# Kernel optimization log

Hardware: AMD Instinct MI355X
Metric: run time of the kernel (lower is better)

The kernel has to match this reference:

```python
import jax, jax.numpy as jnp
import numpy as np

N_NODES = 100000
N_EDGES = 1600000
F_IN, F_HID, F_OUT = 128, 128, 40


def setup_inputs() -> dict:
    key = jax.random.key(0)
    ks = jax.random.split(key, 8)
    x = jax.random.normal(ks[0], (N_NODES, F_IN), dtype=jnp.float32)
    edge_index = jax.random.randint(ks[1], (2, N_EDGES), 0, N_NODES, dtype=jnp.int64)
    # GCNConv weights (glorot-style scale); biases zero per bias_init=zeros_
    W0 = jax.random.normal(ks[2], (F_IN, F_HID), dtype=jnp.float32) / np.sqrt(F_IN)
    b0 = jnp.zeros((F_HID,), dtype=jnp.float32)
    W1 = jax.random.normal(ks[3], (F_HID, F_HID), dtype=jnp.float32) / np.sqrt(F_HID)
    b1 = jnp.zeros((F_HID,), dtype=jnp.float32)
    W2 = jax.random.normal(ks[4], (F_HID, F_OUT), dtype=jnp.float32) / np.sqrt(F_HID)
    b2 = jnp.zeros((F_OUT,), dtype=jnp.float32)
    return {"x": x, "edge_index": edge_index, "W0": W0, "b0": b0,
            "W1": W1, "b1": b1, "W2": W2, "b2": b2}


def _gcn_conv(h, src, dst, W, b):
    # PyG GCNConv (normalize=False, add_self_loops=False):
    # linear transform, then sum-aggregate source features at destinations.
    h = h @ W                                   # [N, F_out]
    msgs = jnp.take(h, src, axis=0)             # [E, F_out] gather
    agg = jax.ops.segment_sum(msgs, dst, num_segments=N_NODES)  # scatter-add
    return agg + b


def reference(x, edge_index, W0, b0, W1, b1, W2, b2):
    src, dst = edge_index[0], edge_index[1]     # flow: source -> target
    h = jax.nn.relu(_gcn_conv(x, src, dst, W0, b0))
    h = jax.nn.relu(_gcn_conv(h, src, dst, W1, b1))
    out = _gcn_conv(h, src, dst, W2, b2)        # last layer: no activation
    return out
```

## Files before the change

### kernel.cpp

```cpp
#include <hip/hip_runtime.h>


typedef short bf16x8 __attribute__((ext_vector_type(8)));
typedef float f32x4  __attribute__((ext_vector_type(4)));

#define EPB 4096

__device__ __forceinline__ float bflo(unsigned int v) {
  union { float f; unsigned int i; } w; w.i = v << 16; return w.f;
}
__device__ __forceinline__ float bfhi(unsigned int v) {
  union { float f; unsigned int i; } w; w.i = v & 0xffff0000u; return w.f;
}
__device__ __forceinline__ unsigned short f2bf(float f) {
  union { float f; unsigned int i; } w; w.f = f;
  unsigned int b = w.i;
  unsigned int r = (b + 0x7fffu + ((b >> 16) & 1u)) >> 16;
  return (unsigned short)r;
}

__device__ __forceinline__ int edge_at(const void* ei, int is64, long long pos) {
  if (is64) return (int)((const long long*)ei)[pos];
  return ((const int*)ei)[pos];
}

__global__ void k_detect(const int* __restrict__ ei32, int* __restrict__ flag) {
  int tid = threadIdx.x;
  int v = ei32[2 * tid + 1];
  unsigned long long m = __ballot(v != 0);
  if (tid == 0) flag[0] = (m == 0ull) ? 1 : 0;
}

__global__ void k_cvt(const float* __restrict__ in, unsigned short* __restrict__ out,
                      long long n4) {
  long long i = (long long)blockIdx.x * blockDim.x + threadIdx.x;
  if (i >= n4) return;
  float4 v = *reinterpret_cast<const float4*>(in + i * 4);
  ushort4 o;
  o.x = f2bf(v.x); o.y = f2bf(v.y); o.z = f2bf(v.z); o.w = f2bf(v.w);
  *reinterpret_cast<ushort4*>(out + i * 4) = o;
}

__global__ void k_wt3(const float* __restrict__ W0, const float* __restrict__ W1,
                      const float* __restrict__ W2,
                      unsigned short* __restrict__ Wt0, unsigned short* __restrict__ Wt1,
                      unsigned short* __restrict__ Wt2, int FOUT, int FP3) {
  int idx = blockIdx.x * blockDim.x + threadIdx.x;
  if (idx < 16384) {
    int c = idx >> 7, k = idx & 127;
    Wt0[c * 128 + k] = f2bf(W0[k * 128 + c]);
  } else if (idx < 32768) {
    int t = idx - 16384;
    int c = t >> 7, k = t & 127;
    Wt1[c * 128 + k] = f2bf(W1[k * 128 + c]);
  } else {
    int t = idx - 32768;
    if (t < FP3 * 128) {
      int c = t >> 7, k = t & 127;
      Wt2[c * 128 + k] = (c < FOUT) ? f2bf(W2[k * FOUT + c]) : (unsigned short)0;
    }
  }
}

__global__ __launch_bounds__(256) void b_hist(const void* __restrict__ ei,
                                              const int* __restrict__ flag, int E,
                                              int* __restrict__ bhist,
                                              int NBKT, int NBLKE) {
  __shared__ int h[512];
  int blk = blockIdx.x, tid = threadIdx.x;
  for (int i = tid; i < NBKT; i += 256) h[i] = 0;
  __syncthreads();
  int is64 = flag[0];
  int base = blk * EPB;
  int cnt = min(EPB, E - base);
  for (int i = tid; i < cnt; i += 256) {
    int d = edge_at(ei, is64, (long long)E + base + i);
    atomicAdd(&h[d >> 8], 1);
  }
  __syncthreads();
  for (int i = tid; i < NBKT; i += 256) bhist[i * NBLKE + blk] = h[i];
}

__global__ void k_scan_a(const int* __restrict__ vals, int* __restrict__ lscan,
                         int* __restrict__ partials, int n) {
  __shared__ int sm[256];
  int tid = threadIdx.x;
  int i = blockIdx.x * 256 + tid;
  int v = (i < n) ? vals[i] : 0;
  sm[tid] = v;
  __syncthreads();
  for (int off = 1; off < 256; off <<= 1) {
    int t = (tid >= off) ? sm[tid - off] : 0;
    __syncthreads();
    sm[tid] += t;
    __syncthreads();
  }
  if (i < n) lscan[i] = sm[tid];
  if (tid == 255) partials[blockIdx.x] = sm[255];
}

__global__ void k_scan_b(int* __restrict__ partials, int nb) {
  __shared__ int sm[1024];
  int tid = threadIdx.x;
  int v = (tid < nb) ? partials[tid] : 0;
  sm[tid] = v;
  __syncthreads();
  for (int off = 1; off < 1024; off <<= 1) {
    int t = (tid >= off) ? sm[tid - off] : 0;
    __syncthreads();
    sm[tid] += t;
    __syncthreads();
  }
  if (tid < nb) partials[tid] = sm[tid] - v;
}

__global__ void k_scan_c(const int* __restrict__ lscan, const int* __restrict__ vals,
                         const int* __restrict__ partials, int* __restrict__ scanned,
                         int* __restrict__ bucketPtr, int n, int NBLKE, int NBKT, int E) {
  int i = blockIdx.x * 256 + threadIdx.x;
  if (i >= n) return;
  int v = lscan[i] - vals[i] + partials[blockIdx.x];
  scanned[i] = v;
  int q = i / NBLKE;
  if (i - q * NBLKE == 0) bucketPtr[q] = v;
  if (i == 0) bucketPtr[NBKT] = E;
}

__global__ __launch_bounds__(256) void b_scatter(const void* __restrict__ ei,
                                                 const int* __restrict__ flag, int E,
                                                 const int* __restrict__ scanned,
                                                 uint2* __restrict__ ebuf,
                                                 int NBKT, int NBLKE) {
  __shared__ int base[512];
  int blk = blockIdx.x, tid = threadIdx.x;
  for (int i = tid; i < NBKT; i += 256) base[i] = scanned[i * NBLKE + blk];
  __syncthreads();
  int is64 = flag[0];
  int b0 = blk * EPB;
  int cnt = min(EPB, E - b0);
  for (int i = tid; i < cnt; i += 256) {
    int d = edge_at(ei, is64, (long long)E + b0 + i);
    int s = edge_at(ei, is64, b0 + i);
    int pos = atomicAdd(&base[d >> 8], 1);
    ebuf[pos] = make_uint2((unsigned)d, (unsigned)s);
  }
}

__global__ __launch_bounds__(256) void b_pass2(const uint2* __restrict__ ebuf,
                                               const int* __restrict__ bucketPtr,
                                               int* __restrict__ rowptr,
                                               int* __restrict__ colsrc,
                                               int N, int NBKT, int E) {
  __shared__ int hist[256], excl[256], cur[256], sm[256];
  int b = blockIdx.x, tid = threadIdx.x;
  hist[tid] = 0;
  __syncthreads();
  int beg = bucketPtr[b], end = bucketPtr[b + 1];
  for (int i = beg + tid; i < end; i += 256)
    atomicAdd(&hist[ebuf[i].x & 255], 1);
  __syncthreads();
  int v = hist[tid];
  sm[tid] = v;
  __syncthreads();
  for (int off = 1; off < 256; off <<= 1) {
    int t = (tid >= off) ? sm[tid - off] : 0;
    __syncthreads();
    sm[tid] += t;
    __syncthreads();
  }
  excl[tid] = sm[tid] - v;
  cur[tid] = 0;
  __syncthreads();
  int nb0 = b << 8;
  if (nb0 + tid < N) rowptr[nb0 + tid] = beg + excl[tid];
  if (b == 0 && tid == 0) rowptr[N] = E;
  for (int i = beg + tid; i < end; i += 256) {
    uint2 e2 = ebuf[i];
    int dl = (int)(e2.x & 255u);
    int r = atomicAdd(&cur[dl], 1);
    colsrc[beg + excl[dl] + r] = (int)e2.y;
  }
}

template <int MODE>
__global__ __launch_bounds__(256) void k_fuse(const unsigned int* __restrict__ H,
                                              const int* __restrict__ rowptr,
                                              const int* __restrict__ colsrc,
                                              const unsigned short* __restrict__ Wt,
                                              const float* __restrict__ bias,
                                              const unsigned short* __restrict__ Wt2,
                                              unsigned short* __restrict__ C,
                                              int N, int FP3) {
  __shared__ unsigned int sh[4096];
  int tid = threadIdx.x;
  int w = tid >> 6, l = tid & 63;
  int sub = l >> 4, fl = l & 15;
  int tile = blockIdx.x * 64 + w * 16;
  unsigned int* my = &sh[w * 1024];

  for (int j = 0; j < 16; ++j) {
    int node = tile + j;
    float a[8] = {0.f, 0.f, 0.f, 0.f, 0.f, 0.f, 0.f, 0.f};
    if (node < N) {
      int beg = rowptr[node], end = rowptr[node + 1];
      int i = beg + sub;
      for (; i + 12 < end; i += 16) {
        int s0 = colsrc[i], s1 = colsrc[i + 4], s2 = colsrc[i + 8], s3 = colsrc[i + 12];
        uint4 v0 = *reinterpret_cast<const uint4*>(H + (size_t)s0 * 64 + fl * 4);
        uint4 v1 = *reinterpret_cast<const uint4*>(H + (size_t)s1 * 64 + fl * 4);
        uint4 v2 = *reinterpret_cast<const uint4*>(H + (size_t)s2 * 64 + fl * 4);
        uint4 v3 = *reinterpret_cast<const uint4*>(H + (size_t)s3 * 64 + fl * 4);
        a[0] += (bflo(v0.x) + bflo(v1.x)) + (bflo(v2.x) + bflo(v3.x));
        a[1] += (bfhi(v0.x) + bfhi(v1.x)) + (bfhi(v2.x) + bfhi(v3.x));
        a[2] += (bflo(v0.y) + bflo(v1.y)) + (bflo(v2.y) + bflo(v3.y));
        a[3] += (bfhi(v0.y) + bfhi(v1.y)) + (bfhi(v2.y) + bfhi(v3.y));
        a[4] += (bflo(v0.z) + bflo(v1.z)) + (bflo(v2.z) + bflo(v3.z));
        a[5] += (bfhi(v0.z) + bfhi(v1.z)) + (bfhi(v2.z) + bfhi(v3.z));
        a[6] += (bflo(v0.w) + bflo(v1.w)) + (bflo(v2.w) + bflo(v3.w));
        a[7] += (bfhi(v0.w) + bfhi(v1.w)) + (bfhi(v2.w) + bfhi(v3.w));
      }
      for (; i < end; i += 4) {
        uint4 v = *reinterpret_cast<const uint4*>(H + (size_t)colsrc[i] * 64 + fl * 4);
        a[0] += bflo(v.x); a[1] += bfhi(v.x);
        a[2] += bflo(v.y); a[3] += bfhi(v.y);
        a[4] += bflo(v.z); a[5] += bfhi(v.z);
        a[6] += bflo(v.w); a[7] += bfhi(v.w);
      }
    }
    #pragma unroll
    for (int k = 0; k < 8; ++k) {
      a[k] += __shfl_xor(a[k], 16);
      a[k] += __shfl_xor(a[k], 32);
    }
    if (sub == 0) {
      uint4 o;
      o.x = ((unsigned)f2bf(a[1]) << 16) | f2bf(a[0]);
      o.y = ((unsigned)f2bf(a[3]) << 16) | f2bf(a[2]);
      o.z = ((unsigned)f2bf(a[5]) << 16) | f2bf(a[4]);
      o.w = ((unsigned)f2bf(a[7]) << 16) | f2bf(a[6]);
      *reinterpret_cast<uint4*>(&my[j * 64 + ((fl ^ j) << 2)]) = o;
    }
  }

  int n = fl;
  bf16x8 af[4];
  #pragma unroll
  for (int ks = 0; ks < 4; ++ks) {
    int c = (ks << 2) | sub;
    af[ks] = *reinterpret_cast<const bf16x8*>(&my[n * 64 + ((c ^ n) << 2)]);
  }
  int kk = sub * 8;
  int ccol = fl;

  if (MODE == 0) {
    #pragma unroll
    for (int cf = 0; cf < 8; ++cf) {
      f32x4 acc = {0.f, 0.f, 0.f, 0.f};
      const unsigned short* wp = Wt + (size_t)(cf * 16 + ccol) * 128 + kk;
      #pragma unroll
      for (int ks = 0; ks < 4; ++ks) {
        bf16x8 b = *reinterpret_cast<const bf16x8*>(wp + ks * 32);
        acc = __builtin_amdgcn_mfma_f32_16x16x32_bf16(af[ks], b, acc, 0, 0, 0);
      }
      float bv = bias[cf * 16 + ccol];
      #pragma unroll
      for (int r = 0; r < 4; ++r) {
        int gr = tile + sub * 4 + r;
        if (gr < N) {
          float v = fmaxf(acc[r] + bv, 0.f);
          C[(size_t)gr * 128 + cf * 16 + ccol] = f2bf(v);
        }
      }
    }
  } else {
    unsigned short* sh16 = (unsigned short*)my;
    #pragma unroll
    for (int cf = 0; cf < 8; ++cf) {
      f32x4 acc = {0.f, 0.f, 0.f, 0.f};
      const unsigned short* wp = Wt + (size_t)(cf * 16 + ccol) * 128 + kk;
      #pragma unroll
      for (int ks = 0; ks < 4; ++ks) {
        bf16x8 b = *reinterpret_cast<const bf16x8*>(wp + ks * 32);
        acc = __builtin_amdgcn_mfma_f32_16x16x32_bf16(af[ks], b, acc, 0, 0, 0);
      }
      float bv = bias[cf * 16 + ccol];
      int col = cf * 16 + ccol;
      int chunk = col >> 3;
      #pragma unroll
      for (int r = 0; r < 4; ++r) {
        int row = sub * 4 + r;
        float v = fmaxf(acc[r] + bv, 0.f);
        sh16[row * 128 + ((chunk ^ row) << 3) + (col & 7)] = f2bf(v);
      }
    }
    bf16x8 af3[4];
    #pragma unroll
    for (int ks = 0; ks < 4; ++ks) {
      int c = (ks << 2) | sub;
      af3[ks] = *reinterpret_cast<const bf16x8*>(&sh16[n * 128 + ((c ^ n) << 3)]);
    }
    for (int cf = 0; cf < FP3 / 16; ++cf) {
      f32x4 acc = {0.f, 0.f, 0.f, 0.f};
      const unsigned short* wp = Wt2 + (size_t)(cf * 16 + ccol) * 128 + kk;
      #pragma unroll
      for (int ks = 0; ks < 4; ++ks) {
        bf16x8 b = *reinterpret_cast<const bf16x8*>(wp + ks * 32);
        acc = __builtin_amdgcn_mfma_f32_16x16x32_bf16(af3[ks], b, acc, 0, 0, 0);
      }
      #pragma unroll
      for (int r = 0; r < 4; ++r) {
        int gr = tile + sub * 4 + r;
        if (gr < N)
          C[(size_t)gr * FP3 + cf * 16 + ccol] = f2bf(acc[r]);
      }
    }
  }
}

__global__ void k_agg40(const unsigned int* __restrict__ T,
                        const int* __restrict__ rowptr, const int* __restrict__ colsrc,
                        const float* __restrict__ b2, float* __restrict__ out, int N) {
  int node = blockIdx.x * 4 + (threadIdx.x >> 6);
  if (node >= N) return;
  int l = threadIdx.x & 63;
  int sub = l >> 4, fl = l & 15;
  int beg = rowptr[node], end = rowptr[node + 1];
  float a[4] = {0.f, 0.f, 0.f, 0.f};
  if (fl < 12) {
    int i = beg + sub;
    for (; i + 12 < end; i += 16) {
      int s0 = colsrc[i], s1 = colsrc[i + 4], s2 = colsrc[i + 8], s3 = colsrc[i + 12];
      uint2 v0 = *reinterpret_cast<const uint2*>(T + (size_t)s0 * 24 + fl * 2);
      uint2 v1 = *reinterpret_cast<const uint2*>(T + (size_t)s1 * 24 + fl * 2);
      uint2 v2 = *reinterpret_cast<const uint2*>(T + (size_t)s2 * 24 + fl * 2);
      uint2 v3 = *reinterpret_cast<const uint2*>(T + (size_t)s3 * 24 + fl * 2);
      a[0] += (bflo(v0.x) + bflo(v1.x)) + (bflo(v2.x) + bflo(v3.x));
      a[1] += (bfhi(v0.x) + bfhi(v1.x)) + (bfhi(v2.x) + bfhi(v3.x));
      a[2] += (bflo(v0.y) + bflo(v1.y)) + (bflo(v2.y) + bflo(v3.y));
      a[3] += (bfhi(v0.y) + bfhi(v1.y)) + (bfhi(v2.y) + bfhi(v3.y));
    }
    for (; i < end; i += 4) {
      uint2 v = *reinterpret_cast<const uint2*>(T + (size_t)colsrc[i] * 24 + fl * 2);
      a[0] += bflo(v.x); a[1] += bfhi(v.x);
      a[2] += bflo(v.y); a[3] += bfhi(v.y);
    }
  }
  #pragma unroll
  for (int k = 0; k < 4; ++k) {
    a[k] += __shfl_xor(a[k], 16);
    a[k] += __shfl_xor(a[k], 32);
  }
  if (sub == 0 && fl < 10) {
    float4 o;
    o.x = a[0] + b2[fl * 4 + 0];
    o.y = a[1] + b2[fl * 4 + 1];
    o.z = a[2] + b2[fl * 4 + 2];
    o.w = a[3] + b2[fl * 4 + 3];
    *reinterpret_cast<float4*>(out + (size_t)node * 40 + fl * 4) = o;
  }
}

extern "C" void kernel_launch(void* const* d_in, const int* in_sizes, int n_in,
                              void* d_out, int out_size, void* d_ws, size_t ws_size,
                              hipStream_t stream) {
  const float* x  = (const float*)d_in[0];
  const void*  ei = d_in[1];
  const float* W0 = (const float*)d_in[2];
  const float* b0 = (const float*)d_in[3];
  const float* W1 = (const float*)d_in[4];
  const float* b1 = (const float*)d_in[5];
  const float* W2 = (const float*)d_in[6];
  const float* b2 = (const float*)d_in[7];
  float* out = (float*)d_out;

  const int N = in_sizes[0] / 128;
  const int E = in_sizes[1] / 2;
  const int FOUT = in_sizes[6] / 128;
  const int FP3 = 48;

  const int NBLKE = (E + EPB - 1) / EPB;
  const int NBKT  = (N + 255) / 256;
  const int T     = NBKT * NBLKE;
  const int GS    = (T + 255) / 256;

  char* wp = (char*)d_ws;
  auto alloc = [&](size_t bytes) -> void* {
    void* p = (void*)wp;
    wp += (bytes + 255) & ~(size_t)255;
    return p;
  };
  unsigned short* xb   = (unsigned short*)alloc((size_t)N * 128 * 2);
  unsigned short* bufH = (unsigned short*)alloc((size_t)N * 128 * 2);
  unsigned short* t3   = (unsigned short*)alloc((size_t)N * FP3 * 2);
  unsigned short* Wt0  = (unsigned short*)alloc(128 * 128 * 2);
  unsigned short* Wt1  = (unsigned short*)alloc(128 * 128 * 2);
  unsigned short* Wt2  = (unsigned short*)alloc(FP3 * 128 * 2);
  uint2* ebuf   = (uint2*)alloc((size_t)E * 8);
  int* colsrc   = (int*)alloc((size_t)E * 4);
  int* rowptr   = (int*)alloc((size_t)(N + 1) * 4);
  int* bhist    = (int*)alloc((size_t)T * 4);
  int* lscan    = (int*)alloc((size_t)T * 4);
  int* scanned  = (int*)alloc((size_t)T * 4);
  int* partials = (int*)alloc(4096);
  int* bucketPtr= (int*)alloc((size_t)(NBKT + 1) * 4);
  int* flag     = (int*)alloc(256);

  k_detect<<<1, 64, 0, stream>>>((const int*)ei, flag);
  long long n4 = (long long)N * 32;
  k_cvt<<<(int)((n4 + 255) / 256), 256, 0, stream>>>(x, xb, n4);
  k_wt3<<<(32768 + FP3 * 128 + 255) / 256, 256, 0, stream>>>(W0, W1, W2, Wt0, Wt1, Wt2,
                                                             FOUT, FP3);
  b_hist<<<NBLKE, 256, 0, stream>>>(ei, flag, E, bhist, NBKT, NBLKE);
  k_scan_a<<<GS, 256, 0, stream>>>(bhist, lscan, partials, T);
  k_scan_b<<<1, 1024, 0, stream>>>(partials, GS);
  k_scan_c<<<GS, 256, 0, stream>>>(lscan, bhist, partials, scanned, bucketPtr,
                                   T, NBLKE, NBKT, E);
  b_scatter<<<NBLKE, 256, 0, stream>>>(ei, flag, E, scanned, ebuf, NBKT, NBLKE);
  b_pass2<<<NBKT, 256, 0, stream>>>(ebuf, bucketPtr, rowptr, colsrc, N, NBKT, E);

  int gfuse = (N + 63) / 64;
  k_fuse<0><<<gfuse, 256, 0, stream>>>((const unsigned int*)xb, rowptr, colsrc,
                                       Wt0, b0, nullptr, bufH, N, FP3);
  k_fuse<1><<<gfuse, 256, 0, stream>>>((const unsigned int*)bufH, rowptr, colsrc,
                                       Wt1, b1, Wt2, t3, N, FP3);
  k_agg40<<<(N + 3) / 4, 256, 0, stream>>>((const unsigned int*)t3, rowptr, colsrc,
                                           b2, out, N);
}
```

Measured before the change: 317.2 us.

## Split fused aggregate+GEMM into separate kernels, merge prep kernels, pack edge buffer

Several changes land together. The fused gather-aggregate-then-MFMA kernels are split into a standalone per-node aggregation kernel plus separate GEMM kernels, which costs an extra round trip of the hidden activations through memory. The detect, convert, weight-transpose and histogram kernels are merged into one prep launch, with int64 detection done per block instead of in a separate kernel. The bucket edge buffer is packed into 32 bits (24-bit source plus 8-bit local dst), which assumes fewer than 16M nodes, and EPB is doubled. The third-layer tensor is padded from 48 to 64 columns so the final aggregation needs no lane masking.

```diff
diff --git a/kernel.cpp b/kernel.cpp
--- a/kernel.cpp
+++ b/kernel.cpp
@@ -4,7 +4,7 @@
 typedef short bf16x8 __attribute__((ext_vector_type(8)));
 typedef float f32x4  __attribute__((ext_vector_type(4)));
 
-#define EPB 4096
+#define EPB 8192
 
 __device__ __forceinline__ float bflo(unsigned int v) {
   union { float f; unsigned int i; } w; w.i = v << 16; return w.f;
@@ -24,61 +24,72 @@
   return ((const int*)ei)[pos];
 }
 
-__global__ void k_detect(const int* __restrict__ ei32, int* __restrict__ flag) {
-  int tid = threadIdx.x;
-  int v = ei32[2 * tid + 1];
-  unsigned long long m = __ballot(v != 0);
-  if (tid == 0) flag[0] = (m == 0ull) ? 1 : 0;
-}
-
-__global__ void k_cvt(const float* __restrict__ in, unsigned short* __restrict__ out,
-                      long long n4) {
-  long long i = (long long)blockIdx.x * blockDim.x + threadIdx.x;
-  if (i >= n4) return;
-  float4 v = *reinterpret_cast<const float4*>(in + i * 4);
-  ushort4 o;
-  o.x = f2bf(v.x); o.y = f2bf(v.y); o.z = f2bf(v.z); o.w = f2bf(v.w);
-  *reinterpret_cast<ushort4*>(out + i * 4) = o;
-}
-
-__global__ void k_wt3(const float* __restrict__ W0, const float* __restrict__ W1,
-                      const float* __restrict__ W2,
-                      unsigned short* __restrict__ Wt0, unsigned short* __restrict__ Wt1,
-                      unsigned short* __restrict__ Wt2, int FOUT, int FP3) {
-  int idx = blockIdx.x * blockDim.x + threadIdx.x;
-  if (idx < 16384) {
-    int c = idx >> 7, k = idx & 127;
-    Wt0[c * 128 + k] = f2bf(W0[k * 128 + c]);
-  } else if (idx < 32768) {
-    int t = idx - 16384;
-    int c = t >> 7, k = t & 127;
-    Wt1[c * 128 + k] = f2bf(W1[k * 128 + c]);
+__device__ __forceinline__ int detect64(const void* ei, int* s_is64, int tid) {
+  if (tid < 64) {
+    int v = ((const int*)ei)[2 * tid + 1];
+    unsigned long long m = __ballot(v != 0);
+    if (tid == 0) *s_is64 = (m == 0ull) ? 1 : 0;
+  }
+  __syncthreads();
+  return *s_is64;
+}
+
+__global__ __launch_bounds__(256) void k_prep(const void* __restrict__ ei, int E,
+                                              int* __restrict__ bhist,
+                                              int NBKT, int NBLKE,
+                                              const float* __restrict__ x,
+                                              unsigned short* __restrict__ xb,
+                                              long long n4, int ncvt,
+                                              const float* __restrict__ W0,
+                                              const float* __restrict__ W1,
+                                              const float* __restrict__ W2,
+                                              unsigned short* __restrict__ Wt0,
+                                              unsigned short* __restrict__ Wt1,
+                                              unsigned short* __restrict__ Wt2,
+                                              int FOUT) {
+  int blk = blockIdx.x, tid = threadIdx.x;
+  if (blk < NBLKE) {
+    __shared__ int h[512];
+    __shared__ int s_is64;
+    if (tid < 64) {
+      int v = ((const int*)ei)[2 * tid + 1];
+      unsigned long long m = __ballot(v != 0);
+      if (tid == 0) s_is64 = (m == 0ull) ? 1 : 0;
+    }
+    for (int i = tid; i < NBKT; i += 256) h[i] = 0;
+    __syncthreads();
+    int is64 = s_is64;
+    int base = blk * EPB;
+    int cnt = min(EPB, E - base);
+    for (int i = tid; i < cnt; i += 256) {
+      int d = edge_at(ei, is64, (long long)E + base + i);
+      atomicAdd(&h[d >> 8], 1);
+    }
+    __syncthreads();
+    for (int i = tid; i < NBKT; i += 256) bhist[i * NBLKE + blk] = h[i];
+  } else if (blk < NBLKE + ncvt) {
+    long long i = (long long)(blk - NBLKE) * 256 + tid;
+    if (i < n4) {
+      float4 v = *reinterpret_cast<const float4*>(x + i * 4);
+      ushort4 o;
+      o.x = f2bf(v.x); o.y = f2bf(v.y); o.z = f2bf(v.z); o.w = f2bf(v.w);
+      *reinterpret_cast<ushort4*>(xb + i * 4) = o;
+    }
   } else {
-    int t = idx - 32768;
-    if (t < FP3 * 128) {
+    int idx = (blk - NBLKE - ncvt) * 256 + tid;
+    if (idx < 16384) {
+      int c = idx >> 7, k = idx & 127;
+      Wt0[c * 128 + k] = f2bf(W0[k * 128 + c]);
+    } else if (idx < 32768) {
+      int t = idx - 16384;
+      int c = t >> 7, k = t & 127;
+      Wt1[c * 128 + k] = f2bf(W1[k * 128 + c]);
+    } else if (idx < 32768 + 8192) {
+      int t = idx - 32768;
       int c = t >> 7, k = t & 127;
       Wt2[c * 128 + k] = (c < FOUT) ? f2bf(W2[k * FOUT + c]) : (unsigned short)0;
     }
   }
-}
-
-__global__ __launch_bounds__(256) void b_hist(const void* __restrict__ ei,
-                                              const int* __restrict__ flag, int E,
-                                              int* __restrict__ bhist,
-                                              int NBKT, int NBLKE) {
-  __shared__ int h[512];
-  int blk = blockIdx.x, tid = threadIdx.x;
-  for (int i = tid; i < NBKT; i += 256) h[i] = 0;
-  __syncthreads();
-  int is64 = flag[0];
-  int base = blk * EPB;
-  int cnt = min(EPB, E - base);
-  for (int i = tid; i < cnt; i += 256) {
-    int d = edge_at(ei, is64, (long long)E + base + i);
-    atomicAdd(&h[d >> 8], 1);
-  }
-  __syncthreads();
-  for (int i = tid; i < NBKT; i += 256) bhist[i * NBLKE + blk] = h[i];
 }
 
 __global__ void k_scan_a(const int* __restrict__ vals, int* __restrict__ lscan,
@@ -126,27 +137,32 @@
   if (i == 0) bucketPtr[NBKT] = E;
 }
 
-__global__ __launch_bounds__(256) void b_scatter(const void* __restrict__ ei,
-                                                 const int* __restrict__ flag, int E,
+__global__ __launch_bounds__(256) void b_scatter(const void* __restrict__ ei, int E,
                                                  const int* __restrict__ scanned,
-                                                 uint2* __restrict__ ebuf,
+                                                 unsigned* __restrict__ ebuf,
                                                  int NBKT, int NBLKE) {
   __shared__ int base[512];
+  __shared__ int s_is64;
   int blk = blockIdx.x, tid = threadIdx.x;
+  if (tid < 64) {
+    int v = ((const int*)ei)[2 * tid + 1];
+    unsigned long long m = __ballot(v != 0);
+    if (tid == 0) s_is64 = (m == 0ull) ? 1 : 0;
+  }
   for (int i = tid; i < NBKT; i += 256) base[i] = scanned[i * NBLKE + blk];
   __syncthreads();
-  int is64 = flag[0];
+  int is64 = s_is64;
   int b0 = blk * EPB;
   int cnt = min(EPB, E - b0);
   for (int i = tid; i < cnt; i += 256) {
     int d = edge_at(ei, is64, (long long)E + b0 + i);
     int s = edge_at(ei, is64, b0 + i);
     int pos = atomicAdd(&base[d >> 8], 1);
-    ebuf[pos] = make_uint2((unsigned)d, (unsigned)s);
-  }
-}
-
-__global__ __launch_bounds__(256) void b_pass2(const uint2* __restrict__ ebuf,
+    ebuf[pos] = (unsigned)s | ((unsigned)(d & 255) << 24);
+  }
+}
+
+__global__ __launch_bounds__(256) void b_pass2(const unsigned* __restrict__ ebuf,
                                                const int* __restrict__ bucketPtr,
                                                int* __restrict__ rowptr,
                                                int* __restrict__ colsrc,
@@ -157,7 +173,7 @@
   __syncthreads();
   int beg = bucketPtr[b], end = bucketPtr[b + 1];
   for (int i = beg + tid; i < end; i += 256)
-    atomicAdd(&hist[ebuf[i].x & 255], 1);
+    atomicAdd(&hist[ebuf[i] >> 24], 1);
   __syncthreads();
   int v = hist[tid];
   sm[tid] = v;
@@ -175,145 +191,57 @@
   if (nb0 + tid < N) rowptr[nb0 + tid] = beg + excl[tid];
   if (b == 0 && tid == 0) rowptr[N] = E;
   for (int i = beg + tid; i < end; i += 256) {
-    uint2 e2 = ebuf[i];
-    int dl = (int)(e2.x & 255u);
+    unsigned e2 = ebuf[i];
+    int dl = (int)(e2 >> 24);
     int r = atomicAdd(&cur[dl], 1);
-    colsrc[beg + excl[dl] + r] = (int)e2.y;
-  }
-}
-
-template <int MODE>
-__global__ __launch_bounds__(256) void k_fuse(const unsigned int* __restrict__ H,
-                                              const int* __restrict__ rowptr,
-                                              const int* __restrict__ colsrc,
-                                              const unsigned short* __restrict__ Wt,
-                                              const float* __restrict__ bias,
-                                              const unsigned short* __restrict__ Wt2,
-                                              unsigned short* __restrict__ C,
-                                              int N, int FP3) {
-  __shared__ unsigned int sh[4096];
-  int tid = threadIdx.x;
-  int w = tid >> 6, l = tid & 63;
+    colsrc[beg + excl[dl] + r] = (int)(e2 & 0xFFFFFFu);
+  }
+}
+
+__global__ void k_agg128b(const unsigned int* __restrict__ H,
+                          const int* __restrict__ rowptr, const int* __restrict__ colsrc,
+                          unsigned int* __restrict__ out, int N) {
+  int node = blockIdx.x * 4 + (threadIdx.x >> 6);
+  if (node >= N) return;
+  int l = threadIdx.x & 63;
   int sub = l >> 4, fl = l & 15;
-  int tile = blockIdx.x * 64 + w * 16;
-  unsigned int* my = &sh[w * 1024];
-
-  for (int j = 0; j < 16; ++j) {
-    int node = tile + j;
-    float a[8] = {0.f, 0.f, 0.f, 0.f, 0.f, 0.f, 0.f, 0.f};
-    if (node < N) {
-      int beg = rowptr[node], end = rowptr[node + 1];
-      int i = beg + sub;
-      for (; i + 12 < end; i += 16) {
-        int s0 = colsrc[i], s1 = colsrc[i + 4], s2 = colsrc[i + 8], s3 = colsrc[i + 12];
-        uint4 v0 = *reinterpret_cast<const uint4*>(H + (size_t)s0 * 64 + fl * 4);
-        uint4 v1 = *reinterpret_cast<const uint4*>(H + (size_t)s1 * 64 + fl * 4);
-        uint4 v2 = *reinterpret_cast<const uint4*>(H + (size_t)s2 * 64 + fl * 4);
-        uint4 v3 = *reinterpret_cast<const uint4*>(H + (size_t)s3 * 64 + fl * 4);
-        a[0] += (bflo(v0.x) + bflo(v1.x)) + (bflo(v2.x) + bflo(v3.x));
-        a[1] += (bfhi(v0.x) + bfhi(v1.x)) + (bfhi(v2.x) + bfhi(v3.x));
-        a[2] += (bflo(v0.y) + bflo(v1.y)) + (bflo(v2.y) + bflo(v3.y));
-        a[3] += (bfhi(v0.y) + bfhi(v1.y)) + (bfhi(v2.y) + bfhi(v3.y));
-        a[4] += (bflo(v0.z) + bflo(v1.z)) + (bflo(v2.z) + bflo(v3.z));
-        a[5] += (bfhi(v0.z) + bfhi(v1.z)) + (bfhi(v2.z) + bfhi(v3.z));
-        a[6] += (bflo(v0.w) + bflo(v1.w)) + (bflo(v2.w) + bflo(v3.w));
-        a[7] += (bfhi(v0.w) + bfhi(v1.w)) + (bfhi(v2.w) + bfhi(v3.w));
-      }
-      for (; i < end; i += 4) {
-        uint4 v = *reinterpret_cast<const uint4*>(H + (size_t)colsrc[i] * 64 + fl * 4);
-        a[0] += bflo(v.x); a[1] += bfhi(v.x);
-        a[2] += bflo(v.y); a[3] += bfhi(v.y);
-        a[4] += bflo(v.z); a[5] += bfhi(v.z);
-        a[6] += bflo(v.w); a[7] += bfhi(v.w);
-      }
-    }
-    #pragma unroll
-    for (int k = 0; k < 8; ++k) {
-      a[k] += __shfl_xor(a[k], 16);
-      a[k] += __shfl_xor(a[k], 32);
-    }
-    if (sub == 0) {
-      uint4 o;
-      o.x = ((unsigned)f2bf(a[1]) << 16) | f2bf(a[0]);
-      o.y = ((unsigned)f2bf(a[3]) << 16) | f2bf(a[2]);
-      o.z = ((unsigned)f2bf(a[5]) << 16) | f2bf(a[4]);
-      o.w = ((unsigned)f2bf(a[7]) << 16) | f2bf(a[6]);
-      *reinterpret_cast<uint4*>(&my[j * 64 + ((fl ^ j) << 2)]) = o;
-    }
-  }
-
-  int n = fl;
-  bf16x8 af[4];
+  int beg = rowptr[node], end = rowptr[node + 1];
+  float a[8] = {0.f, 0.f, 0.f, 0.f, 0.f, 0.f, 0.f, 0.f};
+  int i = beg + sub;
+  for (; i + 12 < end; i += 16) {
+    int s0 = colsrc[i], s1 = colsrc[i + 4], s2 = colsrc[i + 8], s3 = colsrc[i + 12];
+    uint4 v0 = *reinterpret_cast<const uint4*>(H + (size_t)s0 * 64 + fl * 4);
+    uint4 v1 = *reinterpret_cast<const uint4*>(H + (size_t)s1 * 64 + fl * 4);
+    uint4 v2 = *reinterpret_cast<const uint4*>(H + (size_t)s2 * 64 + fl * 4);
+    uint4 v3 = *reinterpret_cast<const uint4*>(H + (size_t)s3 * 64 + fl * 4);
+    a[0] += (bflo(v0.x) + bflo(v1.x)) + (bflo(v2.x) + bflo(v3.x));
+    a[1] += (bfhi(v0.x) + bfhi(v1.x)) + (bfhi(v2.x) + bfhi(v3.x));
+    a[2] += (bflo(v0.y) + bflo(v1.y)) + (bflo(v2.y) + bflo(v3.y));
+    a[3] += (bfhi(v0.y) + bfhi(v1.y)) + (bfhi(v2.y) + bfhi(v3.y));
+    a[4] += (bflo(v0.z) + bflo(v1.z)) + (bflo(v2.z) + bflo(v3.z));
+    a[5] += (bfhi(v0.z) + bfhi(v1.z)) + (bfhi(v2.z) + bfhi(v3.z));
+    a[6] += (bflo(v0.w) + bflo(v1.w)) + (bflo(v2.w) + bflo(v3.w));
+    a[7] += (bfhi(v0.w) + bfhi(v1.w)) + (bfhi(v2.w) + bfhi(v3.w));
+  }
+  for (; i < end; i += 4) {
+    uint4 v = *reinterpret_cast<const uint4*>(H + (size_t)colsrc[i] * 64 + fl * 4);
+    a[0] += bflo(v.x); a[1] += bfhi(v.x);
+    a[2] += bflo(v.y); a[3] += bfhi(v.y);
+    a[4] += bflo(v.z); a[5] += bfhi(v.z);
+    a[6] += bflo(v.w); a[7] += bfhi(v.w);
+  }
   #pragma unroll
-  for (int ks = 0; ks < 4; ++ks) {
-    int c = (ks << 2) | sub;
-    af[ks] = *reinterpret_cast<const bf16x8*>(&my[n * 64 + ((c ^ n) << 2)]);
-  }
-  int kk = sub * 8;
-  int ccol = fl;
-
-  if (MODE == 0) {
-    #pragma unroll
-    for (int cf = 0; cf < 8; ++cf) {
-      f32x4 acc = {0.f, 0.f, 0.f, 0.f};
-      const unsigned short* wp = Wt + (size_t)(cf * 16 + ccol) * 128 + kk;
-      #pragma unroll
-      for (int ks = 0; ks < 4; ++ks) {
-        bf16x8 b = *reinterpret_cast<const bf16x8*>(wp + ks * 32);
-        acc = __builtin_amdgcn_mfma_f32_16x16x32_bf16(af[ks], b, acc, 0, 0, 0);
-      }
-      float bv = bias[cf * 16 + ccol];
-      #pragma unroll
-      for (int r = 0; r < 4; ++r) {
-        int gr = tile + sub * 4 + r;
-        if (gr < N) {
-          float v = fmaxf(acc[r] + bv, 0.f);
-          C[(size_t)gr * 128 + cf * 16 + ccol] = f2bf(v);
-        }
-      }
-    }
-  } else {
-    unsigned short* sh16 = (unsigned short*)my;
-    #pragma unroll
-    for (int cf = 0; cf < 8; ++cf) {
-      f32x4 acc = {0.f, 0.f, 0.f, 0.f};
-      const unsigned short* wp = Wt + (size_t)(cf * 16 + ccol) * 128 + kk;
-      #pragma unroll
-      for (int ks = 0; ks < 4; ++ks) {
-        bf16x8 b = *reinterpret_cast<const bf16x8*>(wp + ks * 32);
-        acc = __builtin_amdgcn_mfma_f32_16x16x32_bf16(af[ks], b, acc, 0, 0, 0);
-      }
-      float bv = bias[cf * 16 + ccol];
-      int col = cf * 16 + ccol;
-      int chunk = col >> 3;
-      #pragma unroll
-      for (int r = 0; r < 4; ++r) {
-        int row = sub * 4 + r;
-        float v = fmaxf(acc[r] + bv, 0.f);
-        sh16[row * 128 + ((chunk ^ row) << 3) + (col & 7)] = f2bf(v);
-      }
-    }
-    bf16x8 af3[4];
-    #pragma unroll
-    for (int ks = 0; ks < 4; ++ks) {
-      int c = (ks << 2) | sub;
-      af3[ks] = *reinterpret_cast<const bf16x8*>(&sh16[n * 128 + ((c ^ n) << 3)]);
-    }
-    for (int cf = 0; cf < FP3 / 16; ++cf) {
-      f32x4 acc = {0.f, 0.f, 0.f, 0.f};
-      const unsigned short* wp = Wt2 + (size_t)(cf * 16 + ccol) * 128 + kk;
-      #pragma unroll
-      for (int ks = 0; ks < 4; ++ks) {
-        bf16x8 b = *reinterpret_cast<const bf16x8*>(wp + ks * 32);
-        acc = __builtin_amdgcn_mfma_f32_16x16x32_bf16(af3[ks], b, acc, 0, 0, 0);
-      }
-      #pragma unroll
-      for (int r = 0; r < 4; ++r) {
-        int gr = tile + sub * 4 + r;
-        if (gr < N)
-          C[(size_t)gr * FP3 + cf * 16 + ccol] = f2bf(acc[r]);
-      }
-    }
+  for (int k = 0; k < 8; ++k) {
+    a[k] += __shfl_xor(a[k], 16);
+    a[k] += __shfl_xor(a[k], 32);
+  }
+  if (sub == 0) {
+    uint4 o;
+    o.x = ((unsigned)f2bf(a[1]) << 16) | f2bf(a[0]);
+    o.y = ((unsigned)f2bf(a[3]) << 16) | f2bf(a[2]);
+    o.z = ((unsigned)f2bf(a[5]) << 16) | f2bf(a[4]);
+    o.w = ((unsigned)f2bf(a[7]) << 16) | f2bf(a[6]);
+    *reinterpret_cast<uint4*>(out + (size_t)node * 64 + fl * 4) = o;
   }
 }
 
@@ -326,24 +254,22 @@
   int sub = l >> 4, fl = l & 15;
   int beg = rowptr[node], end = rowptr[node + 1];
   float a[4] = {0.f, 0.f, 0.f, 0.f};
-  if (fl < 12) {
-    int i = beg + sub;
-    for (; i + 12 < end; i += 16) {
-      int s0 = colsrc[i], s1 = colsrc[i + 4], s2 = colsrc[i + 8], s3 = colsrc[i + 12];
-      uint2 v0 = *reinterpret_cast<const uint2*>(T + (size_t)s0 * 24 + fl * 2);
-      uint2 v1 = *reinterpret_cast<const uint2*>(T + (size_t)s1 * 24 + fl * 2);
-      uint2 v2 = *reinterpret_cast<const uint2*>(T + (size_t)s2 * 24 + fl * 2);
-      uint2 v3 = *reinterpret_cast<const uint2*>(T + (size_t)s3 * 24 + fl * 2);
-      a[0] += (bflo(v0.x) + bflo(v1.x)) + (bflo(v2.x) + bflo(v3.x));
-      a[1] += (bfhi(v0.x) + bfhi(v1.x)) + (bfhi(v2.x) + bfhi(v3.x));
-      a[2] += (bflo(v0.y) + bflo(v1.y)) + (bflo(v2.y) + bflo(v3.y));
-      a[3] += (bfhi(v0.y) + bfhi(v1.y)) + (bfhi(v2.y) + bfhi(v3.y));
-    }
-    for (; i < end; i += 4) {
-      uint2 v = *reinterpret_cast<const uint2*>(T + (size_t)colsrc[i] * 24 + fl * 2);
-      a[0] += bflo(v.x); a[1] += bfhi(v.x);
-      a[2] += bflo(v.y); a[3] += bfhi(v.y);
-    }
+  int i = beg + sub;
+  for (; i + 12 < end; i += 16) {
+    int s0 = colsrc[i], s1 = colsrc[i + 4], s2 = colsrc[i + 8], s3 = colsrc[i + 12];
+    uint2 v0 = *reinterpret_cast<const uint2*>(T + (size_t)s0 * 32 + fl * 2);
+    uint2 v1 = *reinterpret_cast<const uint2*>(T + (size_t)s1 * 32 + fl * 2);
+    uint2 v2 = *reinterpret_cast<const uint2*>(T + (size_t)s2 * 32 + fl * 2);
+    uint2 v3 = *reinterpret_cast<const uint2*>(T + (size_t)s3 * 32 + fl * 2);
+    a[0] += (bflo(v0.x) + bflo(v1.x)) + (bflo(v2.x) + bflo(v3.x));
+    a[1] += (bfhi(v0.x) + bfhi(v1.x)) + (bfhi(v2.x) + bfhi(v3.x));
+    a[2] += (bflo(v0.y) + bflo(v1.y)) + (bflo(v2.y) + bflo(v3.y));
+    a[3] += (bfhi(v0.y) + bfhi(v1.y)) + (bfhi(v2.y) + bfhi(v3.y));
+  }
+  for (; i < end; i += 4) {
+    uint2 v = *reinterpret_cast<const uint2*>(T + (size_t)colsrc[i] * 32 + fl * 2);
+    a[0] += bflo(v.x); a[1] += bfhi(v.x);
+    a[2] += bflo(v.y); a[3] += bfhi(v.y);
   }
   #pragma unroll
   for (int k = 0; k < 4; ++k) {
@@ -357,6 +283,91 @@
     o.z = a[2] + b2[fl * 4 + 2];
     o.w = a[3] + b2[fl * 4 + 3];
     *reinterpret_cast<float4*>(out + (size_t)node * 40 + fl * 4) = o;
+  }
+}
+
+template <int CHAIN>
+__global__ __launch_bounds__(256) void k_gemm(const unsigned short* __restrict__ A,
+                                              const unsigned short* __restrict__ Wt,
+                                              const float* __restrict__ bias,
+                                              const unsigned short* __restrict__ Wt2,
+                                              unsigned short* __restrict__ C, int N) {
+  __shared__ unsigned short sh16[CHAIN ? 4 * 2048 : 64];
+  int tid = threadIdx.x;
+  int w = tid >> 6, l = tid & 63;
+  int sub = l >> 4, fl = l & 15;
+  int r0 = blockIdx.x * 64 + w * 16;
+  int arow = r0 + fl;
+  if (arow >= N) arow = N - 1;
+  int kk = sub * 8;
+  bf16x8 af[4];
+  #pragma unroll
+  for (int ks = 0; ks < 4; ++ks)
+    af[ks] = *reinterpret_cast<const bf16x8*>(A + (size_t)arow * 128 + ks * 32 + kk);
+
+  int ccol = fl;
+  int crow0 = r0 + sub * 4;
+
+  if (CHAIN == 0) {
+    #pragma unroll
+    for (int cf = 0; cf < 8; ++cf) {
+      f32x4 acc = {0.f, 0.f, 0.f, 0.f};
+      const unsigned short* wp = Wt + (size_t)(cf * 16 + ccol) * 128 + kk;
+      #pragma unroll
+      for (int ks = 0; ks < 4; ++ks) {
+        bf16x8 b = *reinterpret_cast<const bf16x8*>(wp + ks * 32);
+        acc = __builtin_amdgcn_mfma_f32_16x16x32_bf16(af[ks], b, acc, 0, 0, 0);
+      }
+      float bv = bias[cf * 16 + ccol];
+      #pragma unroll
+      for (int r = 0; r < 4; ++r) {
+        int gr = crow0 + r;
+        if (gr < N)
+          C[(size_t)gr * 128 + cf * 16 + ccol] = f2bf(fmaxf(acc[r] + bv, 0.f));
+      }
+    }
+  } else {
+    unsigned short* my = &sh16[w * 2048];
+    #pragma unroll
+    for (int cf = 0; cf < 8; ++cf) {
+      f32x4 acc = {0.f, 0.f, 0.f, 0.f};
+      const unsigned short* wp = Wt + (size_t)(cf * 16 + ccol) * 128 + kk;
+      #pragma unroll
+      for (int ks = 0; ks < 4; ++ks) {
+        bf16x8 b = *reinterpret_cast<const bf16x8*>(wp + ks * 32);
+        acc = __builtin_amdgcn_mfma_f32_16x16x32_bf16(af[ks], b, acc, 0, 0, 0);
+      }
+      float bv = bias[cf * 16 + ccol];
+      int col = cf * 16 + ccol;
+      int chunk = col >> 3;
+      #pragma unroll
+      for (int r = 0; r < 4; ++r) {
+        int row = sub * 4 + r;
+        my[row * 128 + ((chunk ^ row) << 3) + (col & 7)] = f2bf(fmaxf(acc[r] + bv, 0.f));
+      }
+    }
+    bf16x8 af3[4];
+    #pragma unroll
+    for (int ks = 0; ks < 4; ++ks) {
+      int c = ks * 4 + sub;
+      af3[ks] = *reinterpret_cast<const bf16x8*>(&my[fl * 128 + ((c ^ fl) << 3)]);
+    }
+    #pragma unroll
+    for (int cf = 0; cf < 4; ++cf) {
+      f32x4 acc = {0.f, 0.f, 0.f, 0.f};
+      const unsigned short* wp = Wt2 + (size_t)(cf * 16 + ccol) * 128 + kk;
+      #pragma unroll
+      for (int ks = 0; ks < 4; ++ks) {
+        bf16x8 b = *reinterpret_cast<const bf16x8*>(wp + ks * 32);
+        acc = __builtin_amdgcn_mfma_f32_16x16x32_bf16(af3[ks], b, acc, 0, 0, 0);
+      }
+      #pragma unroll
+      for (int r = 0; r < 4; ++r) {
+        int gr = crow0 + r;
+        if (gr < N)
+          C[(size_t)gr * 64 + cf * 16 + ccol] = f2bf(acc[r]);
+      }
+    }
   }
 }
 
@@ -376,7 +387,6 @@
   const int N = in_sizes[0] / 128;
   const int E = in_sizes[1] / 2;
   const int FOUT = in_sizes[6] / 128;
-  const int FP3 = 48;
 
   const int NBLKE = (E + EPB - 1) / EPB;
   const int NBKT  = (N + 255) / 256;
@@ -390,12 +400,13 @@
     return p;
   };
   unsigned short* xb   = (unsigned short*)alloc((size_t)N * 128 * 2);
+  unsigned short* bufA = (unsigned short*)alloc((size_t)N * 128 * 2);
   unsigned short* bufH = (unsigned short*)alloc((size_t)N * 128 * 2);
-  unsigned short* t3   = (unsigned short*)alloc((size_t)N * FP3 * 2);
+  unsigned short* t3   = (unsigned short*)alloc((size_t)N * 64 * 2);
   unsigned short* Wt0  = (unsigned short*)alloc(128 * 128 * 2);
   unsigned short* Wt1  = (unsigned short*)alloc(128 * 128 * 2);
-  unsigned short* Wt2  = (unsigned short*)alloc(FP3 * 128 * 2);
-  uint2* ebuf   = (uint2*)alloc((size_t)E * 8);
+  unsigned short* Wt2  = (unsigned short*)alloc(64 * 128 * 2);
+  unsigned* ebuf = (unsigned*)alloc((size_t)E * 4);
   int* colsrc   = (int*)alloc((size_t)E * 4);
   int* rowptr   = (int*)alloc((size_t)(N + 1) * 4);
   int* bhist    = (int*)alloc((size_t)T * 4);
@@ -403,26 +414,29 @@
   int* scanned  = (int*)alloc((size_t)T * 4);
   int* partials = (int*)alloc(4096);
   int* bucketPtr= (int*)alloc((size_t)(NBKT + 1) * 4);
-  int* flag     = (int*)alloc(256);
-
-  k_detect<<<1, 64, 0, stream>>>((const int*)ei, flag);
+
   long long n4 = (long long)N * 32;
-  k_cvt<<<(int)((n4 + 255) / 256), 256, 0, stream>>>(x, xb, n4);
-  k_wt3<<<(32768 + FP3 * 128 + 255) / 256, 256, 0, stream>>>(W0, W1, W2, Wt0, Wt1, Wt2,
-                                                             FOUT, FP3);
-  b_hist<<<NBLKE, 256, 0, stream>>>(ei, flag, E, bhist, NBKT, NBLKE);
+  int ncvt = (int)((n4 + 255) / 256);
+  int nwt  = (32768 + 8192 + 255) / 256;
+
+  k_prep<<<NBLKE + ncvt + nwt, 256, 0, stream>>>(ei, E, bhist, NBKT, NBLKE,
+                                                 x, xb, n4, ncvt,
+                                                 W0, W1, W2, Wt0, Wt1, Wt2, FOUT);
   k_scan_a<<<GS, 256, 0, stream>>>(bhist, lscan, partials, T);
   k_scan_b<<<1, 1024, 0, stream>>>(partials, GS);
   k_scan_c<<<GS, 256, 0, stream>>>(lscan, bhist, partials, scanned, bucketPtr,
                                    T, NBLKE, NBKT, E);
-  b_scatter<<<NBLKE, 256, 0, stream>>>(ei, flag, E, scanned, ebuf, NBKT, NBLKE);
+  b_scatter<<<NBLKE, 256, 0, stream>>>(ei, E, scanned, ebuf, NBKT, NBLKE);
   b_pass2<<<NBKT, 256, 0, stream>>>(ebuf, bucketPtr, rowptr, colsrc, N, NBKT, E);
 
-  int gfuse = (N + 63) / 64;
-  k_fuse<0><<<gfuse, 256, 0, stream>>>((const unsigned int*)xb, rowptr, colsrc,
-                                       Wt0, b0, nullptr, bufH, N, FP3);
-  k_fuse<1><<<gfuse, 256, 0, stream>>>((const unsigned int*)bufH, rowptr, colsrc,
-                                       Wt1, b1, Wt2, t3, N, FP3);
-  k_agg40<<<(N + 3) / 4, 256, 0, stream>>>((const unsigned int*)t3, rowptr, colsrc,
-                                           b2, out, N);
-}
+  int gagg = (N + 3) / 4;
+  int ggemm = (N + 63) / 64;
+  k_agg128b<<<gagg, 256, 0, stream>>>((const unsigned int*)xb, rowptr, colsrc,
+                                      (unsigned int*)bufA, N);
+  k_gemm<0><<<ggemm, 256, 0, stream>>>(bufA, Wt0, b0, nullptr, bufH, N);
+  k_agg128b<<<gagg, 256, 0, stream>>>((const unsigned int*)bufH, rowptr, colsrc,
+                                      (unsigned int*)bufA, N);
+  k_gemm<1><<<ggemm, 256, 0, stream>>>(bufA, Wt1, b1, Wt2, t3, N);
+  k_agg40<<<gagg, 256, 0, stream>>>((const unsigned int*)t3, rowptr, colsrc,
+                                    b2, out, N);
+}
```

Result: faster. 305.4 us (-3.7%).
